# Kernel tuning notes

Hardware: AMD Instinct MI355X
Metric: run time of the kernel (lower is better)

The kernel has to match this reference:

```python
import jax, jax.numpy as jnp
import numpy as np

B, C, T = 256, 8, 1000
PATCH, D, SEQ = 20, 192, 400
N_LAYERS, HEADS = 8, 3
DH = D // HEADS  # 64
HID = 4 * D      # 768
NCLS = 7


def fq(x, n=127.0):
    """Symmetric per-tensor int8 fake-quant (brevitas Int8*PerTensorFloat) with STE."""
    s = jnp.max(jnp.abs(x)) / n + 1e-8
    q = jnp.clip(jnp.round(x / s), -n - 1.0, n) * s
    return x + jax.lax.stop_gradient(q - x)


def fq_u(x, n=255.0):
    """Unsigned per-tensor fake-quant for softmax probabilities (integer softmax output)."""
    s = jnp.max(x) / n + 1e-8
    q = jnp.clip(jnp.round(x / s), 0.0, n) * s
    return x + jax.lax.stop_gradient(q - x)


def ln(x, g, b):
    m = x.mean(-1, keepdims=True)
    v = ((x - m) ** 2).mean(-1, keepdims=True)
    return (x - m) * jax.lax.rsqrt(v + 1e-5) * g + b


def setup_inputs() -> dict:
    key = jax.random.key(0)
    ks = jax.random.split(key, 16)
    w = lambda k, shape: (jax.random.normal(k, shape, jnp.float32) * 0.02)
    inp = {
        "x": jax.random.normal(ks[0], (B, 1, C, T), jnp.float32),
        "patch_w": w(ks[1], (D, PATCH)),          # conv kernel [192,1,1,20] squeezed
        "patch_b": jnp.zeros((D,), jnp.float32),
        "ln1_g": jnp.ones((N_LAYERS, D), jnp.float32),
        "ln1_b": jnp.zeros((N_LAYERS, D), jnp.float32),
        "w_qkv": w(ks[2], (N_LAYERS, 3 * D, D)),
        "b_qkv": jnp.zeros((N_LAYERS, 3 * D), jnp.float32),
        "w_o": w(ks[3], (N_LAYERS, D, D)),
        "b_o": jnp.zeros((N_LAYERS, D), jnp.float32),
        "ln2_g": jnp.ones((N_LAYERS, D), jnp.float32),
        "ln2_b": jnp.zeros((N_LAYERS, D), jnp.float32),
        "w1": w(ks[4], (N_LAYERS, HID, D)),
        "b1": jnp.zeros((N_LAYERS, HID), jnp.float32),
        "w2": w(ks[5], (N_LAYERS, D, HID)),
        "b2": jnp.zeros((N_LAYERS, D), jnp.float32),
        "lnf_g": jnp.ones((D,), jnp.float32),
        "lnf_b": jnp.zeros((D,), jnp.float32),
        "clf_w": w(ks[6], (NCLS, D)),
        "clf_b": jnp.zeros((NCLS,), jnp.float32),
    }
    return inp


def reference(x, patch_w, patch_b, ln1_g, ln1_b, w_qkv, b_qkv, w_o, b_o,
              ln2_g, ln2_b, w1, b1, w2, b2, lnf_g, lnf_b, clf_w, clf_b):
    scale = 1.0 / jnp.sqrt(jnp.float32(DH))

    # input quant
    h = fq(x)
    # patch embed: conv (1,20) stride (1,20) == non-overlapping patchify + GEMM
    p = h.reshape(B, C, T // PATCH, PATCH)          # [B,8,50,20]
    emb = jnp.einsum('bcpt,et->bcpe', p, fq(patch_w)) + patch_b
    h = emb.reshape(B, SEQ, D)                      # token = ch*50 + patch, matches conv reshape
    h = fq(h)

    for i in range(N_LAYERS):
        # --- attention ---
        xn = ln(h, ln1_g[i], ln1_b[i])
        qkv = jnp.einsum('bsd,ed->bse', xn, fq(w_qkv[i])) + b_qkv[i]  # [B,S,576]
        q, k, v = jnp.split(qkv, 3, axis=-1)
        q, k, v = fq(q), fq(k), fq(v)
        q = q.reshape(B, SEQ, HEADS, DH).transpose(0, 2, 1, 3)
        k = k.reshape(B, SEQ, HEADS, DH).transpose(0, 2, 1, 3)
        v = v.reshape(B, SEQ, HEADS, DH).transpose(0, 2, 1, 3)
        scores = jnp.einsum('bhsd,bhtd->bhst', q, k) * scale
        scores = fq(scores)
        probs = jax.nn.softmax(scores, axis=-1)
        probs = fq_u(probs)  # integer softmax output (uint8)
        ctx = jnp.einsum('bhst,bhtd->bhsd', probs, v)
        ctx = ctx.transpose(0, 2, 1, 3).reshape(B, SEQ, D)
        ctx = fq(ctx)
        attn = jnp.einsum('bsd,ed->bse', ctx, fq(w_o[i])) + b_o[i]
        attn = fq(attn)
        h = h + attn
        # --- MLP ---
        xn = ln(h, ln2_g[i], ln2_b[i])
        m = jnp.einsum('bsd,hd->bsh', xn, fq(w1[i])) + b1[i]
        m = fq(jax.nn.gelu(m, approximate=False))
        m = jnp.einsum('bsh,dh->bsd', m, fq(w2[i])) + b2[i]
        m = fq(m)
        h = h + m

    h = ln(h, lnf_g, lnf_b)
    pooled = fq(h.mean(axis=1))                      # [B,192]
    logits = jnp.einsum('bd,cd->bc', pooled, fq(clf_w)) + clf_b
    return logits
```

## Files before the change

kernel.cpp:

```cpp
#include <hip/hip_runtime.h>
#include <math.h>


typedef unsigned int u32;
typedef unsigned short u16;
typedef __attribute__((ext_vector_type(4))) int int4v;

#define MFMA_I8(a, b, c) __builtin_amdgcn_mfma_i32_16x16x64_i8((a), (b), (c), 0, 0, 0)

constexpr int NL = 8;
constexpr long ROWS = 102400;
constexpr float LOG2E = 1.44269504088896340736f;

constexpr int SLOT_X = 0, SLOT_PW = 1, SLOT_EMB = 2, SLOT_CLF = 3, SLOT_POOL = 4;
constexpr int N_SLOT_WORDS = 200 * 16;

constexpr long OFF_GM = 3200;
constexpr long OFF_GL = OFF_GM + 307200;
constexpr long OFF_POOL = OFF_GL + 307200;
constexpr long OFF_PWQ = OFF_POOL + 49152;
constexpr long OFF_CLFQ = OFF_PWQ + 3840;
constexpr long OFF_H = OFF_CLFQ + 1344;
constexpr long OFF_A = OFF_H + 19660800;
constexpr long OFF_U = OFF_A + 19660800;

__device__ __forceinline__ float warpMax(float v) {
#pragma unroll
  for (int o = 32; o > 0; o >>= 1) v = fmaxf(v, __shfl_down(v, o));
  return v;
}

__device__ __forceinline__ float read_max16(const u32* sc, int slot) {
  const u32* p = sc + slot * 16;
  u32 m = 0;
#pragma unroll
  for (int i = 0; i < 16; ++i) m = max(m, p[i]);
  return __uint_as_float(m);
}

__device__ __forceinline__ float fqs(float x, float s) {
  return fminf(fmaxf(rintf(x / s), -128.0f), 127.0f) * s;
}

__global__ void k_zero(u32* p, int n) {
  int i = blockIdx.x * blockDim.x + threadIdx.x;
  if (i < n) p[i] = 0u;
}

__global__ __launch_bounds__(256) void k_absmax(const float4* __restrict__ x, long n4,
                                                u32* __restrict__ slot) {
  float m = 0.f;
  for (long i = (long)blockIdx.x * blockDim.x + threadIdx.x; i < n4;
       i += (long)gridDim.x * blockDim.x) {
    float4 v = x[i];
    m = fmaxf(m, fmaxf(fmaxf(fabsf(v.x), fabsf(v.y)), fmaxf(fabsf(v.z), fabsf(v.w))));
  }
  __shared__ float red[4];
  m = warpMax(m);
  int lane = threadIdx.x & 63, w = threadIdx.x >> 6;
  if (lane == 0) red[w] = m;
  __syncthreads();
  if (threadIdx.x == 0) {
    float r = fmaxf(fmaxf(red[0], red[1]), fmaxf(red[2], red[3]));
    atomicMax(slot + (blockIdx.x & 15), __float_as_uint(r));
  }
}

__global__ __launch_bounds__(256) void k_quant4(const float4* __restrict__ in,
                                                float4* __restrict__ out, long n4,
                                                const u32* __restrict__ sc, int slot) {
  float s = read_max16(sc, slot) / 127.0f + 1e-8f;
  for (long i = (long)blockIdx.x * blockDim.x + threadIdx.x; i < n4;
       i += (long)gridDim.x * blockDim.x) {
    float4 v = in[i];
    v.x = fqs(v.x, s); v.y = fqs(v.y, s); v.z = fqs(v.z, s); v.w = fqs(v.w, s);
    out[i] = v;
  }
}

__global__ __launch_bounds__(256) void k_quant_codes(const float4* __restrict__ in,
                                                     u32* __restrict__ out, long n4,
                                                     const u32* __restrict__ sc, int slot) {
  float s = read_max16(sc, slot) / 127.0f + 1e-8f;
  for (long i = (long)blockIdx.x * blockDim.x + threadIdx.x; i < n4;
       i += (long)gridDim.x * blockDim.x) {
    float4 v = in[i];
    int c0 = (int)fminf(fmaxf(rintf(v.x / s), -128.f), 127.f);
    int c1 = (int)fminf(fmaxf(rintf(v.y / s), -128.f), 127.f);
    int c2 = (int)fminf(fmaxf(rintf(v.z / s), -128.f), 127.f);
    int c3 = (int)fminf(fmaxf(rintf(v.w / s), -128.f), 127.f);
    out[i] = (u32)(c0 & 0xff) | ((u32)(c1 & 0xff) << 8) | ((u32)(c2 & 0xff) << 16) |
             ((u32)(c3 & 0xff) << 24);
  }
}

__global__ __launch_bounds__(192) void k_patch(const float* __restrict__ x,
                                               const float* __restrict__ pwq,
                                               const float* __restrict__ pb,
                                               const u32* __restrict__ sc,
                                               float* __restrict__ emb,
                                               u32* __restrict__ embSlot) {
  __shared__ float xq[8][20];
  __shared__ float red[3];
  const int tid = threadIdx.x;
  const long rowBase = (long)blockIdx.x * 8;
  const float sx = read_max16(sc, SLOT_X) / 127.0f + 1e-8f;
  if (tid < 160) {
    int r = tid / 20, k = tid % 20;
    xq[r][k] = fqs(x[(rowBase + r) * 20 + k], sx);
  }
  __syncthreads();
  float wreg[20];
#pragma unroll
  for (int k = 0; k < 20; ++k) wreg[k] = pwq[tid * 20 + k];
  const float bias = pb[tid];
  float m = 0.f;
  for (int r = 0; r < 8; ++r) {
    float acc = bias;
#pragma unroll
    for (int k = 0; k < 20; ++k) acc += xq[r][k] * wreg[k];
    emb[(rowBase + r) * 192 + tid] = acc;
    m = fmaxf(m, fabsf(acc));
  }
  m = warpMax(m);
  if ((tid & 63) == 0) red[tid >> 6] = m;
  __syncthreads();
  if (tid == 0)
    atomicMax(embSlot + (blockIdx.x & 15),
              __float_as_uint(fmaxf(fmaxf(red[0], red[1]), red[2])));
}

template <bool I16>
__global__ __launch_bounds__(256) void k_ln(const float* __restrict__ x,
                                            const float* __restrict__ g,
                                            const float* __restrict__ bta,
                                            signed char* __restrict__ yh,
                                            signed char* __restrict__ yl,
                                            float* __restrict__ sArow,
                                            float* __restrict__ yf, int rows) {
  int w = threadIdx.x >> 6, lane = threadIdx.x & 63;
  long row = (long)blockIdx.x * 4 + w;
  if (row >= rows) return;
  const bool act = lane < 48;
  float4 v = make_float4(0.f, 0.f, 0.f, 0.f);
  if (act) v = ((const float4*)(x + row * 192))[lane];
  float s = v.x + v.y + v.z + v.w;
#pragma unroll
  for (int o = 32; o > 0; o >>= 1) s += __shfl_down(s, o);
  s = __shfl(s, 0);
  float mean = s / 192.0f;
  float d0 = v.x - mean, d1 = v.y - mean, d2 = v.z - mean, d3 = v.w - mean;
  float q = act ? (d0 * d0 + d1 * d1 + d2 * d2 + d3 * d3) : 0.f;
#pragma unroll
  for (int o = 32; o > 0; o >>= 1) q += __shfl_down(q, o);
  q = __shfl(q, 0);
  float rs = 1.0f / sqrtf(q / 192.0f + 1e-5f);
  float4 gv = make_float4(0.f, 0.f, 0.f, 0.f), bv = gv;
  if (act) {
    gv = ((const float4*)g)[lane];
    bv = ((const float4*)bta)[lane];
  }
  float o0 = d0 * rs * gv.x + bv.x;
  float o1 = d1 * rs * gv.y + bv.y;
  float o2 = d2 * rs * gv.z + bv.z;
  float o3 = d3 * rs * gv.w + bv.w;
  if (I16) {
    float rm = act ? fmaxf(fmaxf(fabsf(o0), fabsf(o1)), fmaxf(fabsf(o2), fabsf(o3))) : 0.f;
#pragma unroll
    for (int o = 32; o > 0; o >>= 1) rm = fmaxf(rm, __shfl_down(rm, o));
    rm = __shfl(rm, 0);
    float sA = rm / 32512.0f + 1e-20f;
    float inv = 1.0f / sA;
    if (act) {
      int c0 = (int)rintf(o0 * inv), c1 = (int)rintf(o1 * inv);
      int c2 = (int)rintf(o2 * inv), c3 = (int)rintf(o3 * inv);
      int h0 = (c0 + 128) >> 8, h1 = (c1 + 128) >> 8;
      int h2 = (c2 + 128) >> 8, h3 = (c3 + 128) >> 8;
      int l0 = c0 - (h0 << 8), l1 = c1 - (h1 << 8);
      int l2 = c2 - (h2 << 8), l3 = c3 - (h3 << 8);
      u32 hw = (u32)(h0 & 0xff) | ((u32)(h1 & 0xff) << 8) | ((u32)(h2 & 0xff) << 16) |
               ((u32)(h3 & 0xff) << 24);
      u32 lw = (u32)(l0 & 0xff) | ((u32)(l1 & 0xff) << 8) | ((u32)(l2 & 0xff) << 16) |
               ((u32)(l3 & 0xff) << 24);
      ((u32*)yh)[row * 48 + lane] = hw;
      ((u32*)yl)[row * 48 + lane] = lw;
    }
    if (lane == 0) sArow[row] = sA;
  } else {
    if (act) ((float4*)(yf + row * 192))[lane] = make_float4(o0, o1, o2, o3);
  }
}

__global__ __launch_bounds__(256) void k_wquant(const float4* __restrict__ w,
                                                u32* __restrict__ out, int n4,
                                                const u32* __restrict__ sc, int slot) {
  int i = blockIdx.x * blockDim.x + threadIdx.x;
  if (i >= n4) return;
  float s = read_max16(sc, slot) / 127.0f + 1e-8f;
  float4 v = w[i];
  int c0 = (int)fminf(fmaxf(rintf(v.x / s), -128.f), 127.f);
  int c1 = (int)fminf(fmaxf(rintf(v.y / s), -128.f), 127.f);
  int c2 = (int)fminf(fmaxf(rintf(v.z / s), -128.f), 127.f);
  int c3 = (int)fminf(fmaxf(rintf(v.w / s), -128.f), 127.f);
  out[i] = (u32)(c0 & 0xff) | ((u32)(c1 & 0xff) << 8) | ((u32)(c2 & 0xff) << 16) |
           ((u32)(c3 & 0xff) << 24);
}

template <bool GELU, int OM>
__global__ __launch_bounds__(256) void k_gemm16(
    const signed char* __restrict__ AH, const signed char* __restrict__ AL,
    const float* __restrict__ sArow, const signed char* __restrict__ W8, int slotW,
    const float* __restrict__ bias, signed char* __restrict__ C8, int N, int ncol,
    u32* __restrict__ sc, int slotO, int colsPerSlot) {
  __shared__ __align__(16) signed char Bs[192 * 208];
  __shared__ float red[4];
  const int tid = threadIdx.x;
  const int bid = blockIdx.x;
  const int vid = (bid & 7) * ((int)gridDim.x >> 3) + (bid >> 3);
  const int bx = vid % ncol;
  const long by = vid / ncol;
  const long rowBase = by * 128;
  const int colBase = bx * 192;
  const float sW = read_max16(sc, slotW) / 127.0f + 1e-8f;

  {
    const signed char* wp = W8 + (long)colBase * 192;
#pragma unroll
    for (int it = 0; it < 9; ++it) {
      int idx = it * 256 + tid;
      int row = idx / 12, c = idx % 12;
      int4 v = *(const int4*)(wp + (long)row * 192 + c * 16);
      *(int4*)&Bs[row * 208 + c * 16] = v;
    }
  }

  const int lane = tid & 63, w = tid >> 6;
  const int fr = lane & 15, fk = lane >> 4;
  const int wc0 = w * 48;

  float sOinv = 0.f;
  if (OM == 2) sOinv = 1.0f / (read_max16(sc, slotO + colBase / colsPerSlot) / 127.0f + 1e-8f);
  const float inv_sqrt2 = 0.70710678118654752440f;
  float vmax = 0.f;

  const long abase = (rowBase + fr) * 192 + fk * 16;
  __syncthreads();

#pragma unroll 1
  for (int it = 0; it < 8; ++it) {
    const long ab = abase + (long)it * 16 * 192;
    int4v ahc[3], alc[3];
#pragma unroll
    for (int kk = 0; kk < 3; ++kk) {
      ahc[kk] = *(const int4v*)(AH + ab + kk * 64);
      alc[kk] = *(const int4v*)(AL + ab + kk * 64);
    }
    int4v aH[3], aL[3];
#pragma unroll
    for (int n = 0; n < 3; ++n) {
      aH[n] = (int4v){0, 0, 0, 0};
      aL[n] = (int4v){0, 0, 0, 0};
    }
#pragma unroll
    for (int kk = 0; kk < 3; ++kk) {
#pragma unroll
      for (int n = 0; n < 3; ++n) {
        int4v bfr = *(const int4v*)&Bs[(wc0 + n * 16 + fr) * 208 + kk * 64 + fk * 16];
        aH[n] = MFMA_I8(ahc[kk], bfr, aH[n]);
        aL[n] = MFMA_I8(alc[kk], bfr, aL[n]);
      }
    }
    const long rt = rowBase + it * 16;
    float4 sA4 = *(const float4*)&sArow[rt + fk * 4];
    float sAr[4] = {sA4.x, sA4.y, sA4.z, sA4.w};
#pragma unroll
    for (int n = 0; n < 3; ++n) {
      const int col = colBase + wc0 + n * 16 + fr;
      const float bb = bias[col];
#pragma unroll
      for (int r = 0; r < 4; ++r) {
        const int R = (aH[n][r] << 8) + aL[n][r];
        float val = (float)R * (sAr[r] * sW) + bb;
        if (GELU) val = 0.5f * val * (1.0f + erff(val * inv_sqrt2));
        if (OM == 2) {
          float code = fminf(fmaxf(rintf(val * sOinv), -128.f), 127.f);
          C8[(rt + fk * 4 + r) * N + col] = (signed char)code;
        } else {
          vmax = fmaxf(vmax, fabsf(val));
        }
      }
    }
  }

  if (OM == 1) {
    float m = warpMax(vmax);
    if ((tid & 63) == 0) red[tid >> 6] = m;
    __syncthreads();
    if (tid == 0) {
      float r = fmaxf(fmaxf(red[0], red[1]), fmaxf(red[2], red[3]));
      atomicMax(sc + (slotO + colBase / colsPerSlot) * 16 + ((int)(bx + by) & 15),
                __float_as_uint(r));
    }
  }
}

template <int OM>
__global__ __launch_bounds__(256) void k_gemm8(
    const signed char* __restrict__ A8, int slotA, const signed char* __restrict__ W8,
    int slotW, const float* __restrict__ bias, float* __restrict__ H, int N, int K,
    u32* __restrict__ sc, int slotO) {
  __shared__ float red[4];
  const int tid = threadIdx.x;
  const long rowBase = (long)blockIdx.y * 128;
  const int colBase = blockIdx.x * 192;
  const float alpha = (read_max16(sc, slotA) / 127.0f + 1e-8f) *
                      (read_max16(sc, slotW) / 127.0f + 1e-8f);

  const int lane = tid & 63, wv = tid >> 6;
  const int wm = wv >> 1, wn = wv & 1;
  const int fr = lane & 15, fk = lane >> 4;

  int4v acc[4][6];
#pragma unroll
  for (int m = 0; m < 4; ++m)
#pragma unroll
    for (int n = 0; n < 6; ++n) acc[m][n] = (int4v){0, 0, 0, 0};

  const long arow0 = rowBase + wm * 64;
  const int bcol0 = colBase + wn * 96;

  for (int k0 = 0; k0 < K; k0 += 64) {
    const int ko = k0 + fk * 16;
    int4v bfr[6];
#pragma unroll
    for (int n = 0; n < 6; ++n)
      bfr[n] = *(const int4v*)(W8 + (long)(bcol0 + n * 16 + fr) * K + ko);
#pragma unroll
    for (int m = 0; m < 4; ++m) {
      int4v af = *(const int4v*)(A8 + (arow0 + m * 16 + fr) * (long)K + ko);
#pragma unroll
      for (int n = 0; n < 6; ++n) acc[m][n] = MFMA_I8(af, bfr[n], acc[m][n]);
    }
  }

  float sO = 1.f;
  if (OM == 3) sO = read_max16(sc, slotO) / 127.0f + 1e-8f;
  float vmax = 0.f;
#pragma unroll
  for (int n = 0; n < 6; ++n) {
    const int col = colBase + wn * 96 + n * 16 + fr;
    const float bb = bias[col];
#pragma unroll
    for (int m = 0; m < 4; ++m) {
#pragma unroll
      for (int r = 0; r < 4; ++r) {
        const long row = rowBase + wm * 64 + m * 16 + fk * 4 + r;
        float val = (float)acc[m][n][r] * alpha + bb;
        if (OM == 3) {
          H[row * N + col] += fqs(val, sO);
        } else {
          vmax = fmaxf(vmax, fabsf(val));
        }
      }
    }
  }
  if (OM == 1) {
    float m = warpMax(vmax);
    if ((tid & 63) == 0) red[tid >> 6] = m;
    __syncthreads();
    if (tid == 0) {
      float r = fmaxf(fmaxf(red[0], red[1]), fmaxf(red[2], red[3]));
      atomicMax(sc + slotO * 16 + ((blockIdx.x + blockIdx.y) & 15), __float_as_uint(r));
    }
  }
}

__global__ __launch_bounds__(256) void k_vt(const signed char* __restrict__ qkv8,
                                            signed char* __restrict__ vt8,
                                            int* __restrict__ colsum) {
  __shared__ __align__(16) signed char T[64 * 80];
  __shared__ int cs[64];
  const int tid = threadIdx.x;
  const int bh = blockIdx.x, b = bh / 3, hh = bh % 3;
  const signed char* vb = qkv8 + (long)b * 400 * 576 + hh * 64 + 384;
  if (tid < 64) cs[tid] = 0;
  const int d = tid >> 2, seg = tid & 3;
  for (int c0 = 0; c0 < 448; c0 += 64) {
    __syncthreads();
    {
      int trow = tid >> 2, c = tid & 3;
      int4 v = make_int4(0, 0, 0, 0);
      if (c0 + trow < 400) v = *(const int4*)(vb + (long)(c0 + trow) * 576 + c * 16);
      *(int4*)&T[trow * 80 + c * 16] = v;
    }
    __syncthreads();
    int4 outw;
    int ssum = 0;
    u32 pk[4];
#pragma unroll
    for (int j = 0; j < 4; ++j) {
      u32 p = 0;
#pragma unroll
      for (int e = 0; e < 4; ++e) {
        int t = seg * 16 + j * 4 + e;
        int v = (int)T[t * 80 + d];
        ssum += v;
        p |= ((u32)(v & 0xff)) << (8 * e);
      }
      pk[j] = p;
    }
    outw.x = (int)pk[0]; outw.y = (int)pk[1]; outw.z = (int)pk[2]; outw.w = (int)pk[3];
    if (c0 + seg * 16 < 400)
      *(int4*)&vt8[(long)bh * 25600 + d * 400 + c0 + seg * 16] = outw;
    atomicAdd(&cs[d], ssum);
  }
  __syncthreads();
  if (tid < 64) colsum[bh * 64 + tid] = cs[tid];
}

__device__ __forceinline__ void attn_swz(int& tile, int& bh) {
  int bid = blockIdx.x;
  int vid = (bid & 7) * ((int)gridDim.x >> 3) + (bid >> 3);
  tile = vid % 7;
  bh = vid / 7;
}

__global__ __launch_bounds__(256) void k_attn0(const signed char* __restrict__ qkv8,
                                               int* __restrict__ gmInt, u32* __restrict__ sc,
                                               int slotQ, int slotSc) {
  __shared__ float red[4];
  const int tid = threadIdx.x;
  int tile, bh;
  attn_swz(tile, bh);
  const int r0 = tile * 64;
  const int b = bh / 3, hh = bh % 3;
  const signed char* qb = qkv8 + (long)b * 400 * 576 + hh * 64;
  const signed char* kb = qb + 192;
  const float sQ = read_max16(sc, slotQ) / 127.0f + 1e-8f;
  const float sK = read_max16(sc, slotQ + 1) / 127.0f + 1e-8f;
  const float sSc = sQ * sK * 0.125f;

  const int lane = tid & 63, w = tid >> 6, fr = lane & 15, fk = lane >> 4;
  const int qloc = 16 * w + fr;
  const int gq = r0 + qloc;
  const bool qv = gq < 400;
  int4v qf = *(const int4v*)(qb + (long)(r0 + qloc) * 576 + fk * 16);

  int aim = 0;
  int rim = -(1 << 30);
  for (int c0 = 0; c0 < 400; c0 += 128) {
#pragma unroll
    for (int tf = 0; tf < 8; ++tf) {
      int4v kf = *(const int4v*)(kb + (long)(c0 + tf * 16 + fr) * 576 + fk * 16);
      int4v s = MFMA_I8(kf, qf, ((int4v){0, 0, 0, 0}));
      const bool tv = (c0 + tf * 16 + fk * 4) < 400;
      if (tv && qv) {
#pragma unroll
        for (int r = 0; r < 4; ++r) {
          int sv = s[r];
          aim = max(aim, max(sv, -sv));
          rim = max(rim, sv);
        }
      }
    }
  }
  rim = max(rim, __shfl_xor(rim, 16));
  rim = max(rim, __shfl_xor(rim, 32));
  if (fk == 0 && qv) gmInt[(long)bh * 400 + gq] = rim;
  float m = warpMax((float)aim * sSc);
  if (lane == 0) red[w] = m;
  __syncthreads();
  if (tid == 0) {
    float r = fmaxf(fmaxf(red[0], red[1]), fmaxf(red[2], red[3]));
    atomicMax(sc + slotSc * 16 + (blockIdx.x & 15), __float_as_uint(r));
  }
}

__global__ __launch_bounds__(256) void k_attn1(const signed char* __restrict__ qkv8,
                                               float* __restrict__ gm, float* __restrict__ gl,
                                               const int* __restrict__ gmInt,
                                               u32* __restrict__ sc, int slotQ, int slotSc,
                                               int slotPr) {
  __shared__ float red[4];
  const int tid = threadIdx.x;
  int tile, bh;
  attn_swz(tile, bh);
  const int r0 = tile * 64;
  const int b = bh / 3, hh = bh % 3;
  const signed char* qb = qkv8 + (long)b * 400 * 576 + hh * 64;
  const signed char* kb = qb + 192;
  const float sQ = read_max16(sc, slotQ) / 127.0f + 1e-8f;
  const float sK = read_max16(sc, slotQ + 1) / 127.0f + 1e-8f;
  const float sSc = sQ * sK * 0.125f;
  const float sS = read_max16(sc, slotSc) / 127.0f + 1e-8f;
  const float c1 = sSc / sS;
  const float c2 = sS * LOG2E;

  const int lane = tid & 63, w = tid >> 6, fr = lane & 15, fk = lane >> 4;
  const int qloc = 16 * w + fr;
  const int gq = r0 + qloc;
  const int gqc = (gq > 399) ? 399 : gq;
  int4v qf = *(const int4v*)(qb + (long)(r0 + qloc) * 576 + fk * 16);

  const int mint = gmInt[(long)bh * 400 + gqc];
  const float cm = fminf(fmaxf(rintf((float)mint * c1), -128.f), 127.f);

  float sum = 0.f;
  for (int c0 = 0; c0 < 400; c0 += 128) {
#pragma unroll
    for (int tf = 0; tf < 8; ++tf) {
      int4v kf = *(const int4v*)(kb + (long)(c0 + tf * 16 + fr) * 576 + fk * 16);
      int4v s = MFMA_I8(kf, qf, ((int4v){0, 0, 0, 0}));
      if ((c0 + tf * 16 + fk * 4) < 400) {
#pragma unroll
        for (int r = 0; r < 4; ++r) {
          float cf = fminf(fmaxf(rintf((float)s[r] * c1), -128.f), 127.f);
          sum += exp2f((cf - cm) * c2);
        }
      }
    }
  }
  sum += __shfl_xor(sum, 16);
  sum += __shfl_xor(sum, 32);
  float cand = 0.f;
  if (fk == 0 && gq < 400) {
    gm[(long)bh * 400 + gq] = cm;
    gl[(long)bh * 400 + gq] = sum;
    cand = 1.0f / sum;
  }
  float m = warpMax(cand);
  if (lane == 0) red[w] = m;
  __syncthreads();
  if (tid == 0) {
    float r = fmaxf(fmaxf(red[0], red[1]), fmaxf(red[2], red[3]));
    atomicMax(sc + slotPr * 16 + (blockIdx.x & 15), __float_as_uint(r));
  }
}

__global__ __launch_bounds__(256) void k_attn_pv(
    const signed char* __restrict__ qkv8, const signed char* __restrict__ vt8,
    const int* __restrict__ colsumV, float* __restrict__ ctx, const float* __restrict__ gm,
    const float* __restrict__ gl, u32* __restrict__ sc, int slotQ, int slotSc, int slotPr,
    int slotCtx) {
  __shared__ __align__(16) signed char Ps[64 * 144];
  __shared__ int colsV[64];
  __shared__ float red[4];
  const int tid = threadIdx.x;
  int tile, bh;
  attn_swz(tile, bh);
  const int r0 = tile * 64;
  const int b = bh / 3, hh = bh % 3;
  const signed char* qb = qkv8 + (long)b * 400 * 576 + hh * 64;
  const signed char* kb = qb + 192;
  const signed char* vtb = vt8 + (long)bh * 25600;
  const float sQ = read_max16(sc, slotQ) / 127.0f + 1e-8f;
  const float sK = read_max16(sc, slotQ + 1) / 127.0f + 1e-8f;
  const float sV = read_max16(sc, slotQ + 2) / 127.0f + 1e-8f;
  const float sSc = sQ * sK * 0.125f;
  const float sS = read_max16(sc, slotSc) / 127.0f + 1e-8f;
  const float sP = read_max16(sc, slotPr) / 255.0f + 1e-8f;
  const float sPV = sP * sV;
  const float c1 = sSc / sS;
  const float c2 = sS * LOG2E;

  if (tid < 64) colsV[tid] = colsumV[bh * 64 + tid];
  const int lane = tid & 63, w = tid >> 6, fr = lane & 15, fk = lane >> 4;
  const int qloc = 16 * w + fr;
  int4v qf = *(const int4v*)(qb + (long)(r0 + qloc) * 576 + fk * 16);

  int gq = r0 + qloc;
  if (gq > 399) gq = 399;
  const float cm = gm[(long)bh * 400 + gq];
  const float invLsp = 1.0f / (gl[(long)bh * 400 + gq] * sP);

  int4v accd[4];
#pragma unroll
  for (int dt = 0; dt < 4; ++dt) accd[dt] = (int4v){0, 0, 0, 0};
  __syncthreads();

  for (int c0 = 0; c0 < 400; c0 += 128) {
#pragma unroll
    for (int tf = 0; tf < 8; ++tf) {
      int4v kf = *(const int4v*)(kb + (long)(c0 + tf * 16 + fr) * 576 + fk * 16);
      int4v s = MFMA_I8(kf, qf, ((int4v){0, 0, 0, 0}));
      const int tbase = c0 + tf * 16 + fk * 4;
      u32 pack = 0;
      if (tbase < 400) {
#pragma unroll
        for (int r = 0; r < 4; ++r) {
          float cf = fminf(fmaxf(rintf((float)s[r] * c1), -128.f), 127.f);
          float e = exp2f((cf - cm) * c2);
          float pu = fminf(fmaxf(rintf(e * invLsp), 0.f), 255.f);
          int pc = (int)pu - 128;
          pack |= ((u32)(pc & 0xff)) << (8 * r);
        }
      }
      *(u32*)&Ps[qloc * 144 + tf * 16 + fk * 4] = pack;
    }
    __syncthreads();
    int4v pf0 = *(const int4v*)&Ps[qloc * 144 + fk * 16];
    int4v pf1 = *(const int4v*)&Ps[qloc * 144 + 64 + fk * 16];
    const bool v0ok = (c0 + fk * 16) < 400;
    const bool v1ok = (c0 + 64 + fk * 16) < 400;
#pragma unroll
    for (int dt = 0; dt < 4; ++dt) {
      const long vrow = (long)(dt * 16 + fr) * 400;
      int4v vf0 = v0ok ? *(const int4v*)(vtb + vrow + c0 + fk * 16) : (int4v){0, 0, 0, 0};
      int4v vf1 = v1ok ? *(const int4v*)(vtb + vrow + c0 + 64 + fk * 16) : (int4v){0, 0, 0, 0};
      accd[dt] = MFMA_I8(vf0, pf0, accd[dt]);
      accd[dt] = MFMA_I8(vf1, pf1, accd[dt]);
    }
    __syncthreads();
  }
  float vmax = 0.f;
  const int q = r0 + qloc;
  if (q < 400) {
#pragma unroll
    for (int dt = 0; dt < 4; ++dt) {
      const int d0 = dt * 16 + fk * 4;
      float4 o;
      o.x = sPV * (float)(accd[dt][0] + 128 * colsV[d0 + 0]);
      o.y = sPV * (float)(accd[dt][1] + 128 * colsV[d0 + 1]);
      o.z = sPV * (float)(accd[dt][2] + 128 * colsV[d0 + 2]);
      o.w = sPV * (float)(accd[dt][3] + 128 * colsV[d0 + 3]);
      vmax = fmaxf(vmax, fmaxf(fmaxf(fabsf(o.x), fabsf(o.y)), fmaxf(fabsf(o.z), fabsf(o.w))));
      *(float4*)&ctx[(long)(b * 400 + q) * 192 + hh * 64 + d0] = o;
    }
  }
  float m = warpMax(vmax);
  if (lane == 0) red[w] = m;
  __syncthreads();
  if (tid == 0) {
    float r = fmaxf(fmaxf(red[0], red[1]), fmaxf(red[2], red[3]));
    atomicMax(sc + slotCtx * 16 + (blockIdx.x & 15), __float_as_uint(r));
  }
}

__global__ __launch_bounds__(192) void k_pool(const float* __restrict__ xln,
                                              float* __restrict__ pooled,
                                              u32* __restrict__ slot) {
  int b = blockIdx.x, d = threadIdx.x;
  float sum = 0.f;
  for (int s = 0; s < 400; ++s) sum += xln[((long)b * 400 + s) * 192 + d];
  float v = sum / 400.0f;
  pooled[(long)b * 192 + d] = v;
  __shared__ float red[3];
  float m = warpMax(fabsf(v));
  if ((d & 63) == 0) red[d >> 6] = m;
  __syncthreads();
  if (d == 0)
    atomicMax(slot + (b & 15), __float_as_uint(fmaxf(fmaxf(red[0], red[1]), red[2])));
}

__global__ __launch_bounds__(64) void k_logits(const float* __restrict__ pooled,
                                               const float* __restrict__ clfq,
                                               const float* __restrict__ clfb,
                                               const u32* __restrict__ sc,
                                               float* __restrict__ out) {
  int c = blockIdx.x, b = blockIdx.y, lane = threadIdx.x;
  float sp = read_max16(sc, SLOT_POOL) / 127.0f + 1e-8f;
  float acc = 0.f;
#pragma unroll
  for (int j = 0; j < 3; ++j) {
    int d = lane + 64 * j;
    acc += fqs(pooled[(long)b * 192 + d], sp) * clfq[c * 192 + d];
  }
#pragma unroll
  for (int o = 32; o > 0; o >>= 1) acc += __shfl_down(acc, o);
  if (lane == 0) out[b * 7 + c] = acc + clfb[c];
}

static inline int gsz(long n4, long cap) {
  long g = (n4 + 255) / 256;
  return (int)(g < cap ? g : cap);
}

extern "C" void kernel_launch(void* const* d_in, const int* in_sizes, int n_in,
                              void* d_out, int out_size, void* d_ws, size_t ws_size,
                              hipStream_t stream) {
  (void)in_sizes; (void)n_in; (void)out_size; (void)ws_size;

  const float* x = (const float*)d_in[0];
  const float* pw = (const float*)d_in[1];
  const float* pb = (const float*)d_in[2];
  const float* ln1g = (const float*)d_in[3];
  const float* ln1b = (const float*)d_in[4];
  const float* wqkv = (const float*)d_in[5];
  const float* bqkv = (const float*)d_in[6];
  const float* wo = (const float*)d_in[7];
  const float* bo = (const float*)d_in[8];
  const float* ln2g = (const float*)d_in[9];
  const float* ln2b = (const float*)d_in[10];
  const float* w1 = (const float*)d_in[11];
  const float* b1 = (const float*)d_in[12];
  const float* w2 = (const float*)d_in[13];
  const float* b2 = (const float*)d_in[14];
  const float* lnfg = (const float*)d_in[15];
  const float* lnfb = (const float*)d_in[16];
  const float* clfw = (const float*)d_in[17];
  const float* clfb = (const float*)d_in[18];

  float* ws = (float*)d_ws;
  u32* sc = (u32*)d_ws;
  float* GM = ws + OFF_GM;
  int* GMI = (int*)GM;
  float* GL = ws + OFF_GL;
  float* POOL = ws + OFF_POOL;
  float* PWQ = ws + OFF_PWQ;
  float* CLFQ = ws + OFF_CLFQ;
  float* H = ws + OFF_H;
  float* Af = ws + OFF_A;
  signed char* AH8 = (signed char*)(ws + OFF_A);
  signed char* AL8 = AH8 + 19660800;
  float* SAROW = (float*)(AH8 + 2 * 19660800);
  signed char* U8 = (signed char*)(ws + OFF_U);
  signed char* VT8 = U8 + 58982400;
  int* COLSUM = (int*)POOL;
  signed char* WQC = (signed char*)POOL;
  signed char* WOC2 = (signed char*)POOL;
  signed char* W1C2 = (signed char*)POOL + 36864;
  signed char* W2C2 = (signed char*)POOL + 36864;
  float* out = (float*)d_out;

  k_zero<<<(N_SLOT_WORDS + 255) / 256, 256, 0, stream>>>(sc, N_SLOT_WORDS);

  auto amax = [&](const float* p, long n, int slot) {
    k_absmax<<<gsz(n / 4, 256), 256, 0, stream>>>((const float4*)p, n / 4, sc + slot * 16);
  };
  amax(pw, 3840, SLOT_PW);
  amax(clfw, 1344, SLOT_CLF);
  amax(x, 2048000, SLOT_X);
  for (int i = 0; i < NL; ++i) {
    int Lb = 16 + i * 16;
    amax(wqkv + (long)i * 110592, 110592, Lb + 0);
    amax(wo + (long)i * 36864, 36864, Lb + 1);
    amax(w1 + (long)i * 147456, 147456, Lb + 2);
    amax(w2 + (long)i * 147456, 147456, Lb + 3);
  }
  k_quant4<<<gsz(960, 256), 256, 0, stream>>>((const float4*)pw, (float4*)PWQ, 960, sc, SLOT_PW);
  k_quant4<<<gsz(336, 256), 256, 0, stream>>>((const float4*)clfw, (float4*)CLFQ, 336, sc,
                                              SLOT_CLF);

  k_patch<<<12800, 192, 0, stream>>>(x, PWQ, pb, sc, Af, sc + SLOT_EMB * 16);
  k_quant4<<<2048, 256, 0, stream>>>((const float4*)Af, (float4*)H, 19660800 / 4, sc, SLOT_EMB);
  k_ln<true><<<(int)(ROWS / 4), 256, 0, stream>>>(H, ln1g, ln1b, AH8, AL8, SAROW, nullptr,
                                                  (int)ROWS);

  for (int i = 0; i < NL; ++i) {
    int Lb = 16 + i * 16;
    k_wquant<<<108, 256, 0, stream>>>((const float4*)(wqkv + (long)i * 110592), (u32*)WQC,
                                      27648, sc, Lb + 0);
    k_gemm16<false, 1><<<2400, 256, 0, stream>>>(AH8, AL8, SAROW, WQC, Lb + 0, bqkv + i * 576,
                                                 nullptr, 576, 3, sc, Lb + 4, 192);
    k_gemm16<false, 2><<<2400, 256, 0, stream>>>(AH8, AL8, SAROW, WQC, Lb + 0, bqkv + i * 576,
                                                 U8, 576, 3, sc, Lb + 4, 192);
    k_vt<<<768, 256, 0, stream>>>(U8, VT8, COLSUM);
    k_attn0<<<5376, 256, 0, stream>>>(U8, GMI, sc, Lb + 4, Lb + 7);
    k_attn1<<<5376, 256, 0, stream>>>(U8, GM, GL, GMI, sc, Lb + 4, Lb + 7, Lb + 8);
    k_attn_pv<<<5376, 256, 0, stream>>>(U8, VT8, COLSUM, Af, GM, GL, sc, Lb + 4, Lb + 7,
                                        Lb + 8, Lb + 9);
    k_quant_codes<<<2048, 256, 0, stream>>>((const float4*)Af, (u32*)U8, 19660800 / 4, sc,
                                            Lb + 9);
    k_wquant<<<36, 256, 0, stream>>>((const float4*)(wo + (long)i * 36864), (u32*)WOC2, 9216,
                                     sc, Lb + 1);
    {
      dim3 g(1, 800);
      k_gemm8<1><<<g, 256, 0, stream>>>(U8, Lb + 9, WOC2, Lb + 1, bo + i * 192, nullptr, 192,
                                        192, sc, Lb + 10);
      k_gemm8<3><<<g, 256, 0, stream>>>(U8, Lb + 9, WOC2, Lb + 1, bo + i * 192, H, 192, 192,
                                        sc, Lb + 10);
    }
    k_ln<true><<<(int)(ROWS / 4), 256, 0, stream>>>(H, ln2g + i * 192, ln2b + i * 192, AH8,
                                                    AL8, SAROW, nullptr, (int)ROWS);
    k_wquant<<<144, 256, 0, stream>>>((const float4*)(w1 + (long)i * 147456), (u32*)W1C2,
                                      36864, sc, Lb + 2);
    k_gemm16<true, 1><<<3200, 256, 0, stream>>>(AH8, AL8, SAROW, W1C2, Lb + 2, b1 + i * 768,
                                                nullptr, 768, 4, sc, Lb + 11, 768);
    k_gemm16<true, 2><<<3200, 256, 0, stream>>>(AH8, AL8, SAROW, W1C2, Lb + 2, b1 + i * 768,
                                                U8, 768, 4, sc, Lb + 11, 768);
    k_wquant<<<144, 256, 0, stream>>>((const float4*)(w2 + (long)i * 147456), (u32*)W2C2,
                                      36864, sc, Lb + 3);
    {
      dim3 g(1, 800);
      k_gemm8<1><<<g, 256, 0, stream>>>(U8, Lb + 11, W2C2, Lb + 3, b2 + i * 192, nullptr, 192,
                                        768, sc, Lb + 12);
      k_gemm8<3><<<g, 256, 0, stream>>>(U8, Lb + 11, W2C2, Lb + 3, b2 + i * 192, H, 192, 768,
                                        sc, Lb + 12);
    }
    if (i < NL - 1) {
      k_ln<true><<<(int)(ROWS / 4), 256, 0, stream>>>(H, ln1g + (i + 1) * 192,
                                                      ln1b + (i + 1) * 192, AH8, AL8, SAROW,
                                                      nullptr, (int)ROWS);
    } else {
      k_ln<false><<<(int)(ROWS / 4), 256, 0, stream>>>(H, lnfg, lnfb, nullptr, nullptr,
                                                       nullptr, Af, (int)ROWS);
    }
  }

  k_pool<<<256, 192, 0, stream>>>(Af, POOL, sc + SLOT_POOL * 16);
  {
    dim3 g(7, 256);
    k_logits<<<g, 64, 0, stream>>>(POOL, CLFQ, clfb, sc, out);
  }
}
```

Before: 6.999 ms.

## Store int8 GEMM output once and fuse residual fake-quant add into LayerNorm

```diff
diff --git a/kernel.cpp b/kernel.cpp
--- a/kernel.cpp
+++ b/kernel.cpp
@@ -100,25 +100,31 @@
                                                const u32* __restrict__ sc,
                                                float* __restrict__ emb,
                                                u32* __restrict__ embSlot) {
-  __shared__ float xq[8][20];
+  __shared__ float wsm[3840];
+  __shared__ float xq[160];
   __shared__ float red[3];
   const int tid = threadIdx.x;
   const long rowBase = (long)blockIdx.x * 8;
   const float sx = read_max16(sc, SLOT_X) / 127.0f + 1e-8f;
-  if (tid < 160) {
-    int r = tid / 20, k = tid % 20;
-    xq[r][k] = fqs(x[(rowBase + r) * 20 + k], sx);
+#pragma unroll
+  for (int j = 0; j < 5; ++j)
+    ((float4*)wsm)[j * 192 + tid] = ((const float4*)pwq)[j * 192 + tid];
+  if (tid < 40) {
+    float4 v = ((const float4*)(x + rowBase * 20))[tid];
+    v.x = fqs(v.x, sx); v.y = fqs(v.y, sx); v.z = fqs(v.z, sx); v.w = fqs(v.w, sx);
+    ((float4*)xq)[tid] = v;
   }
   __syncthreads();
   float wreg[20];
 #pragma unroll
-  for (int k = 0; k < 20; ++k) wreg[k] = pwq[tid * 20 + k];
+  for (int k = 0; k < 20; ++k) wreg[k] = wsm[tid * 20 + k];
   const float bias = pb[tid];
   float m = 0.f;
+#pragma unroll
   for (int r = 0; r < 8; ++r) {
     float acc = bias;
 #pragma unroll
-    for (int k = 0; k < 20; ++k) acc += xq[r][k] * wreg[k];
+    for (int k = 0; k < 20; ++k) acc += xq[r * 20 + k] * wreg[k];
     emb[(rowBase + r) * 192 + tid] = acc;
     m = fmaxf(m, fabsf(acc));
   }
@@ -130,20 +136,31 @@
               __float_as_uint(fmaxf(fmaxf(red[0], red[1]), red[2])));
 }
 
-template <bool I16>
-__global__ __launch_bounds__(256) void k_ln(const float* __restrict__ x,
-                                            const float* __restrict__ g,
-                                            const float* __restrict__ bta,
-                                            signed char* __restrict__ yh,
-                                            signed char* __restrict__ yl,
-                                            float* __restrict__ sArow,
-                                            float* __restrict__ yf, int rows) {
+template <bool RES, bool I16>
+__global__ __launch_bounds__(256) void k_resln(float* __restrict__ H,
+                                               const float* __restrict__ raw,
+                                               const u32* __restrict__ sc, int slotRes,
+                                               const float* __restrict__ g,
+                                               const float* __restrict__ bta,
+                                               signed char* __restrict__ yh,
+                                               signed char* __restrict__ yl,
+                                               float* __restrict__ sArow,
+                                               float* __restrict__ yf, int rows) {
   int w = threadIdx.x >> 6, lane = threadIdx.x & 63;
   long row = (long)blockIdx.x * 4 + w;
   if (row >= rows) return;
   const bool act = lane < 48;
   float4 v = make_float4(0.f, 0.f, 0.f, 0.f);
-  if (act) v = ((const float4*)(x + row * 192))[lane];
+  if (act) v = ((const float4*)(H + row * 192))[lane];
+  if (RES) {
+    float sres = read_max16(sc, slotRes) / 127.0f + 1e-8f;
+    if (act) {
+      float4 r4 = ((const float4*)(raw + row * 192))[lane];
+      v.x += fqs(r4.x, sres); v.y += fqs(r4.y, sres);
+      v.z += fqs(r4.z, sres); v.w += fqs(r4.w, sres);
+      ((float4*)(H + row * 192))[lane] = v;
+    }
+  }
   float s = v.x + v.y + v.z + v.w;
 #pragma unroll
   for (int o = 32; o > 0; o >>= 1) s += __shfl_down(s, o);
@@ -304,10 +321,9 @@
   }
 }
 
-template <int OM>
 __global__ __launch_bounds__(256) void k_gemm8(
     const signed char* __restrict__ A8, int slotA, const signed char* __restrict__ W8,
-    int slotW, const float* __restrict__ bias, float* __restrict__ H, int N, int K,
+    int slotW, const float* __restrict__ bias, float* __restrict__ C, int N, int K,
     u32* __restrict__ sc, int slotO) {
   __shared__ float red[4];
   const int tid = threadIdx.x;
@@ -343,8 +359,6 @@
     }
   }
 
-  float sO = 1.f;
-  if (OM == 3) sO = read_max16(sc, slotO) / 127.0f + 1e-8f;
   float vmax = 0.f;
 #pragma unroll
   for (int n = 0; n < 6; ++n) {
@@ -356,15 +370,12 @@
       for (int r = 0; r < 4; ++r) {
         const long row = rowBase + wm * 64 + m * 16 + fk * 4 + r;
         float val = (float)acc[m][n][r] * alpha + bb;
-        if (OM == 3) {
-          H[row * N + col] += fqs(val, sO);
-        } else {
-          vmax = fmaxf(vmax, fabsf(val));
-        }
+        C[row * N + col] = val;
+        vmax = fmaxf(vmax, fabsf(val));
       }
     }
   }
-  if (OM == 1) {
+  {
     float m = warpMax(vmax);
     if ((tid & 63) == 0) red[tid >> 6] = m;
     __syncthreads();
@@ -709,12 +720,24 @@
   float* PWQ = ws + OFF_PWQ;
   float* CLFQ = ws + OFF_CLFQ;
   float* H = ws + OFF_H;
-  float* Af = ws + OFF_A;
-  signed char* AH8 = (signed char*)(ws + OFF_A);
-  signed char* AL8 = AH8 + 19660800;
-  float* SAROW = (float*)(AH8 + 2 * 19660800);
-  signed char* U8 = (signed char*)(ws + OFF_U);
-  signed char* VT8 = U8 + 58982400;
+
+  signed char* RA = (signed char*)(ws + OFF_A);
+  signed char* RU = (signed char*)(ws + OFF_U);
+  signed char* PLQ_H = RU;
+  signed char* PLQ_L = RU + 19660800;
+  float* PLQ_S = (float*)(RU + 39321600);
+  signed char* QKV8 = RA;
+  signed char* VT8 = RA + 58982400;
+  float* CTXF = (float*)RU;
+  signed char* CTX8 = RA;
+  float* WOOUT = (float*)RU;
+  signed char* PL2_H = RA;
+  signed char* PL2_L = RA + 19660800;
+  float* PL2_S = (float*)(RA + 39321600);
+  signed char* GELU8 = RU;
+  float* W2OUT = (float*)RA;
+  float* FINALF = (float*)RU;
+
   int* COLSUM = (int*)POOL;
   signed char* WQC = (signed char*)POOL;
   signed char* WOC2 = (signed char*)POOL;
@@ -741,63 +764,63 @@
   k_quant4<<<gsz(336, 256), 256, 0, stream>>>((const float4*)clfw, (float4*)CLFQ, 336, sc,
                                               SLOT_CLF);
 
-  k_patch<<<12800, 192, 0, stream>>>(x, PWQ, pb, sc, Af, sc + SLOT_EMB * 16);
-  k_quant4<<<2048, 256, 0, stream>>>((const float4*)Af, (float4*)H, 19660800 / 4, sc, SLOT_EMB);
-  k_ln<true><<<(int)(ROWS / 4), 256, 0, stream>>>(H, ln1g, ln1b, AH8, AL8, SAROW, nullptr,
-                                                  (int)ROWS);
+  k_patch<<<12800, 192, 0, stream>>>(x, PWQ, pb, sc, (float*)RU, sc + SLOT_EMB * 16);
+  k_quant4<<<2048, 256, 0, stream>>>((const float4*)RU, (float4*)H, 19660800 / 4, sc, SLOT_EMB);
+  k_resln<false, true><<<(int)(ROWS / 4), 256, 0, stream>>>(
+      H, nullptr, sc, 0, ln1g, ln1b, PLQ_H, PLQ_L, PLQ_S, nullptr, (int)ROWS);
 
   for (int i = 0; i < NL; ++i) {
     int Lb = 16 + i * 16;
     k_wquant<<<108, 256, 0, stream>>>((const float4*)(wqkv + (long)i * 110592), (u32*)WQC,
                                       27648, sc, Lb + 0);
-    k_gemm16<false, 1><<<2400, 256, 0, stream>>>(AH8, AL8, SAROW, WQC, Lb + 0, bqkv + i * 576,
-                                                 nullptr, 576, 3, sc, Lb + 4, 192);
-    k_gemm16<false, 2><<<2400, 256, 0, stream>>>(AH8, AL8, SAROW, WQC, Lb + 0, bqkv + i * 576,
-                                                 U8, 576, 3, sc, Lb + 4, 192);
-    k_vt<<<768, 256, 0, stream>>>(U8, VT8, COLSUM);
-    k_attn0<<<5376, 256, 0, stream>>>(U8, GMI, sc, Lb + 4, Lb + 7);
-    k_attn1<<<5376, 256, 0, stream>>>(U8, GM, GL, GMI, sc, Lb + 4, Lb + 7, Lb + 8);
-    k_attn_pv<<<5376, 256, 0, stream>>>(U8, VT8, COLSUM, Af, GM, GL, sc, Lb + 4, Lb + 7,
+    k_gemm16<false, 1><<<2400, 256, 0, stream>>>(PLQ_H, PLQ_L, PLQ_S, WQC, Lb + 0,
+                                                 bqkv + i * 576, nullptr, 576, 3, sc, Lb + 4,
+                                                 192);
+    k_gemm16<false, 2><<<2400, 256, 0, stream>>>(PLQ_H, PLQ_L, PLQ_S, WQC, Lb + 0,
+                                                 bqkv + i * 576, QKV8, 576, 3, sc, Lb + 4,
+                                                 192);
+    k_vt<<<768, 256, 0, stream>>>(QKV8, VT8, COLSUM);
+    k_attn0<<<5376, 256, 0, stream>>>(QKV8, GMI, sc, Lb + 4, Lb + 7);
+    k_attn1<<<5376, 256, 0, stream>>>(QKV8, GM, GL, GMI, sc, Lb + 4, Lb + 7, Lb + 8);
+    k_attn_pv<<<5376, 256, 0, stream>>>(QKV8, VT8, COLSUM, CTXF, GM, GL, sc, Lb + 4, Lb + 7,
                                         Lb + 8, Lb + 9);
-    k_quant_codes<<<2048, 256, 0, stream>>>((const float4*)Af, (u32*)U8, 19660800 / 4, sc,
+    k_quant_codes<<<2048, 256, 0, stream>>>((const float4*)CTXF, (u32*)CTX8, 19660800 / 4, sc,
                                             Lb + 9);
     k_wquant<<<36, 256, 0, stream>>>((const float4*)(wo + (long)i * 36864), (u32*)WOC2, 9216,
                                      sc, Lb + 1);
     {
       dim3 g(1, 800);
-      k_gemm8<1><<<g, 256, 0, stream>>>(U8, Lb + 9, WOC2, Lb + 1, bo + i * 192, nullptr, 192,
-                                        192, sc, Lb + 10);
-      k_gemm8<3><<<g, 256, 0, stream>>>(U8, Lb + 9, WOC2, Lb + 1, bo + i * 192, H, 192, 192,
-                                        sc, Lb + 10);
-    }
-    k_ln<true><<<(int)(ROWS / 4), 256, 0, stream>>>(H, ln2g + i * 192, ln2b + i * 192, AH8,
-                                                    AL8, SAROW, nullptr, (int)ROWS);
+      k_gemm8<<<g, 256, 0, stream>>>(CTX8, Lb + 9, WOC2, Lb + 1, bo + i * 192, WOOUT, 192, 192,
+                                     sc, Lb + 10);
+    }
+    k_resln<true, true><<<(int)(ROWS / 4), 256, 0, stream>>>(
+        H, WOOUT, sc, Lb + 10, ln2g + i * 192, ln2b + i * 192, PL2_H, PL2_L, PL2_S, nullptr,
+        (int)ROWS);
     k_wquant<<<144, 256, 0, stream>>>((const float4*)(w1 + (long)i * 147456), (u32*)W1C2,
                                       36864, sc, Lb + 2);
-    k_gemm16<true, 1><<<3200, 256, 0, stream>>>(AH8, AL8, SAROW, W1C2, Lb + 2, b1 + i * 768,
-                                                nullptr, 768, 4, sc, Lb + 11, 768);
-    k_gemm16<true, 2><<<3200, 256, 0, stream>>>(AH8, AL8, SAROW, W1C2, Lb + 2, b1 + i * 768,
-                                                U8, 768, 4, sc, Lb + 11, 768);
+    k_gemm16<true, 1><<<3200, 256, 0, stream>>>(PL2_H, PL2_L, PL2_S, W1C2, Lb + 2,
+                                                b1 + i * 768, nullptr, 768, 4, sc, Lb + 11,
+                                                768);
+    k_gemm16<true, 2><<<3200, 256, 0, stream>>>(PL2_H, PL2_L, PL2_S, W1C2, Lb + 2,
+                                                b1 + i * 768, GELU8, 768, 4, sc, Lb + 11, 768);
     k_wquant<<<144, 256, 0, stream>>>((const float4*)(w2 + (long)i * 147456), (u32*)W2C2,
                                       36864, sc, Lb + 3);
     {
       dim3 g(1, 800);
-      k_gemm8<1><<<g, 256, 0, stream>>>(U8, Lb + 11, W2C2, Lb + 3, b2 + i * 192, nullptr, 192,
-                                        768, sc, Lb + 12);
-      k_gemm8<3><<<g, 256, 0, stream>>>(U8, Lb + 11, W2C2, Lb + 3, b2 + i * 192, H, 192, 768,
-                                        sc, Lb + 12);
+      k_gemm8<<<g, 256, 0, stream>>>(GELU8, Lb + 11, W2C2, Lb + 3, b2 + i * 192, W2OUT, 192,
+                                     768, sc, Lb + 12);
     }
     if (i < NL - 1) {
-      k_ln<true><<<(int)(ROWS / 4), 256, 0, stream>>>(H, ln1g + (i + 1) * 192,
-                                                      ln1b + (i + 1) * 192, AH8, AL8, SAROW,
-                                                      nullptr, (int)ROWS);
+      k_resln<true, true><<<(int)(ROWS / 4), 256, 0, stream>>>(
+          H, W2OUT, sc, Lb + 12, ln1g + (i + 1) * 192, ln1b + (i + 1) * 192, PLQ_H, PLQ_L,
+          PLQ_S, nullptr, (int)ROWS);
     } else {
-      k_ln<false><<<(int)(ROWS / 4), 256, 0, stream>>>(H, lnfg, lnfb, nullptr, nullptr,
-                                                       nullptr, Af, (int)ROWS);
-    }
-  }
-
-  k_pool<<<256, 192, 0, stream>>>(Af, POOL, sc + SLOT_POOL * 16);
+      k_resln<true, false><<<(int)(ROWS / 4), 256, 0, stream>>>(
+          H, W2OUT, sc, Lb + 12, lnfg, lnfb, nullptr, nullptr, nullptr, FINALF, (int)ROWS);
+    }
+  }
+
+  k_pool<<<256, 192, 0, stream>>>(FINALF, POOL, sc + SLOT_POOL * 16);
   {
     dim3 g(7, 256);
     k_logits<<<g, 64, 0, stream>>>(POOL, CLFQ, clfb, sc, out);
```

Measured after the change: 6.070 ms. -13.3%, faster.
